# Kernel optimization log

Measured on AMD Instinct MI355X. Metric: run time of the kernel, lower is better.

Reference implementation:

```python
import jax, jax.numpy as jnp
import numpy as np

TAU = 2.0      # spikingjelly MultiStepLIFNode default tau
VTH = 1.0      # default v_threshold
ALPHA = 4.0    # default Sigmoid surrogate alpha
EPS = 1e-5     # BatchNorm eps

# --- STE sign for binarized conv weights (Binarize.apply, det mode, scale=1) ---
@jax.custom_vjp
def ste_sign(x):
    return jnp.sign(x)

def _ss_fwd(x):
    return jnp.sign(x), None

def _ss_bwd(_, g):
    return (g,)

ste_sign.defvjp(_ss_fwd, _ss_bwd)

# --- Heaviside spike with sigmoid surrogate gradient ---
@jax.custom_vjp
def spike_fn(x):
    return (x >= 0.0).astype(x.dtype)

def _sp_fwd(x):
    return (x >= 0.0).astype(x.dtype), x

def _sp_bwd(x, g):
    s = jax.nn.sigmoid(ALPHA * x)
    return (g * ALPHA * s * (1.0 - s),)

spike_fn.defvjp(_sp_fwd, _sp_bwd)

def lif(x):
    # x: [T,B,C,H,W]; LIF with v_reset=None (soft reset), decay_input=True,
    # detach_reset=True (stop_gradient on the reset term).
    def step(v, xt):
        v = v + (xt - v) / TAU
        s = spike_fn(v - VTH)
        v = v - jax.lax.stop_gradient(s) * VTH
        return v, s
    v0 = jnp.zeros_like(x[0])
    _, spikes = jax.lax.scan(step, v0, x)
    return spikes

def conv3x3(x, w, groups=1):
    # x: [N,C,H,W], w: [O, C//groups, 3, 3], stride 1, pad 1
    return jax.lax.conv_general_dilated(
        x, w, window_strides=(1, 1), padding=((1, 1), (1, 1)),
        dimension_numbers=('NCHW', 'OIHW', 'NCHW'),
        feature_group_count=groups)

def setup_inputs() -> dict:
    key = jax.random.key(0)
    k1, k2, k3 = jax.random.split(key, 3)
    x = jax.random.normal(k1, (4, 8, 256, 64, 64), dtype=jnp.float32)
    w1 = jax.random.normal(k2, (192, 256, 3, 3), dtype=jnp.float32) * 0.05
    gamma = jnp.ones((192,), dtype=jnp.float32)
    beta = jnp.zeros((192,), dtype=jnp.float32)
    w2 = jax.random.normal(k3, (320, 48, 3, 3), dtype=jnp.float32) * 0.05
    return {'x': x, 'w1': w1, 'gamma': gamma, 'beta': beta, 'w2': w2}

def reference(x, w1, gamma, beta, w2):
    T, B, C, H, W = x.shape
    s = lif(x).reshape(T * B, C, H, W)          # spikes, flatten(0,1)
    y = conv3x3(s, w1)                          # conv1 (bias=False)
    # BatchNorm2d in training mode: batch stats over (N,H,W), biased var
    mean = y.mean(axis=(0, 2, 3))
    var = y.var(axis=(0, 2, 3))
    yb = (y - mean[None, :, None, None]) * jax.lax.rsqrt(var + EPS)[None, :, None, None]
    yb = yb * gamma[None, :, None, None] + beta[None, :, None, None]
    hidden = yb.shape[1]
    x1 = yb.reshape(T, B, hidden, H, W)
    z = conv3x3(yb, ste_sign(w2), groups=4)     # binarized-weight conv, groups=4
    x2 = z.reshape(T, B, -1, H, W)
    return jnp.concatenate((x1, x2), axis=2)    # [T,B,output_size,H,W]
```

## Files before the change

kernel.cpp:

```cpp
#include <hip/hip_runtime.h>

typedef __bf16 bf16x8 __attribute__((ext_vector_type(8)));
typedef float f32x4 __attribute__((ext_vector_type(4)));

#define DEV static __device__ __forceinline__

DEV ushort f2bf(float f) {
  unsigned u = __builtin_bit_cast(unsigned, f);
  u = (u + 0x7FFFu + ((u >> 16) & 1u)) >> 16;
  return (ushort)u;
}
DEV float bf2f(ushort h) {
  unsigned u = ((unsigned)h) << 16;
  return __builtin_bit_cast(float, u);
}
DEV void gll16(const void* g, void* l) {
  __builtin_amdgcn_global_load_lds((const __attribute__((address_space(1))) void*)g,
                                   (__attribute__((address_space(3))) void*)l, 16, 0, 0);
}

#define Y_OFF      71368704ull
#define WR1_OFF    121700352ull
#define WR2_OFF    122585088ull
#define STATS_OFF  122953728ull
#define ZERO_OFF   122955264ull
#define PART_OFF   122959360ull

DEV void border_px(int p, int& h, int& w) {
  if (p < 66)       { h = 0;       w = p; }
  else if (p < 132) { h = 65;      w = p - 66; }
  else if (p < 196) { h = p - 131; w = 0; }
  else              { h = p - 195; w = 65; }
}
__global__ void halo1_kernel(ushort* __restrict__ S) {
  const int idx = blockIdx.x * 256 + threadIdx.x;
  const int n = idx / 16640, r = idx % 16640;
  const int p = r >> 6, c4 = r & 63;
  int h, w; border_px(p, h, w);
  ushort4 z; z.x = 0; z.y = 0; z.z = 0; z.w = 0;
  *(ushort4*)&S[((size_t)((n * 66 + h) * 66 + w) << 8) + c4 * 4] = z;
}
__global__ void halo2_kernel(ushort* __restrict__ Yb) {
  const int idx = blockIdx.x * 256 + threadIdx.x;
  const int n = idx / 12480, r = idx % 12480;
  const int p = r / 48, c4 = r % 48;
  int h, w; border_px(p, h, w);
  ushort4 z; z.x = 0; z.y = 0; z.z = 0; z.w = 0;
  *(ushort4*)&Yb[(size_t)((n * 66 + h) * 66 + w) * 192 + c4 * 4] = z;
}

__global__ __launch_bounds__(256) void lif_kernel(const float* __restrict__ x,
                                                  ushort* __restrict__ S) {
  const int bi = blockIdx.x;
  const int jq = bi >> 9;
  const int b  = (bi >> 6) & 7;
  const int h  = bi & 63;
  const int tid = threadIdx.x;
  const int w0 = (tid & 15) << 2;
  const int cg = (tid >> 4) + (jq << 4);
  const int c0 = cg << 2;

  float v[4][4];
#pragma unroll
  for (int a = 0; a < 4; ++a)
#pragma unroll
    for (int k = 0; k < 4; ++k) v[a][k] = 0.f;

#pragma unroll
  for (int t = 0; t < 4; ++t) {
    const int n = t * 8 + b;
    ushort sp[4][4];
#pragma unroll
    for (int a = 0; a < 4; ++a) {
      const float4 xv = *(const float4*)(x + ((size_t)(n * 256 + c0 + a) << 12) + (h << 6) + w0);
      const float xa[4] = {xv.x, xv.y, xv.z, xv.w};
#pragma unroll
      for (int k = 0; k < 4; ++k) {
        v[a][k] += (xa[k] - v[a][k]) * 0.5f;
        const bool s = v[a][k] >= 1.0f;
        sp[a][k] = s ? (ushort)0x3F80 : (ushort)0;
        v[a][k] -= s ? 1.0f : 0.0f;
      }
    }
#pragma unroll
    for (int k = 0; k < 4; ++k) {
      ushort4 o4; o4.x = sp[0][k]; o4.y = sp[1][k]; o4.z = sp[2][k]; o4.w = sp[3][k];
      *(ushort4*)(S + ((size_t)((n * 66 + h + 1) * 66 + (w0 + k + 1)) << 8) + c0) = o4;
    }
  }
}

__global__ void prep_w1_kernel(const float* __restrict__ w1, ushort* __restrict__ Wr1) {
  const int idx = blockIdx.x * 256 + threadIdx.x;
  const int pos = idx / 49152, r = idx % 49152;
  const int o = r >> 8, c = r & 255;
  Wr1[idx] = f2bf(w1[(o * 256 + c) * 9 + pos]);
}
__global__ void prep_w2_kernel(const float* __restrict__ w2, ushort* __restrict__ Wr2) {
  const int idx = blockIdx.x * 256 + threadIdx.x;
  const int gp = idx / 5120, r = idx % 5120;
  const int o = r >> 6, c = r & 63;
  const int g = gp / 9, pos = gp % 9;
  float v = 0.f;
  if (c < 48) {
    const float wv = w2[((g * 80 + o) * 48 + c) * 9 + pos];
    v = (wv > 0.f) ? 1.f : ((wv < 0.f) ? -1.f : 0.f);
  }
  Wr2[idx] = f2bf(v);
}

__global__ __launch_bounds__(256, 2) void conv1_kernel(const ushort* __restrict__ S,
                                                       const ushort* __restrict__ Wr1,
                                                       ushort* __restrict__ Y,
                                                       float* __restrict__ Pp) {
  __shared__ ushort ldsA[2][12288];
  __shared__ ushort ldsB[2][8192];
  const int tid = threadIdx.x;
  const int l = tid & 63, wv = tid >> 6;
  const int wrow = wv >> 1, wcol = wv & 1;
  const int col = l & 15, quad = l >> 4;
  const int bid = ((blockIdx.x & 7) << 7) | (blockIdx.x >> 3);
  const int pxb = bid << 7;
  const int n = pxb >> 12;
  const int h0 = (pxb >> 6) & 63;
  const int n66h0 = n * 66 + h0;

  int goA[6], loA[6];
#pragma unroll
  for (int ii = 0; ii < 6; ++ii) {
    const int s = ii * 256 + tid;
    const int kc = s / 768, r = s % 768;
    const int row = r >> 2, op = r & 3;
    const int ol = (op - (row >> 1)) & 3;
    goA[ii] = row * 256 + kc * 32 + ol * 8;
    loA[ii] = s * 8;
  }
  int goB[4], loB[4];
#pragma unroll
  for (int ii = 0; ii < 4; ++ii) {
    const int s = ii * 256 + tid;
    const int kc = s >> 9, r = s & 511;
    const int pxl = r >> 2, op = r & 3;
    const int ol = (op - (pxl >> 1)) & 3;
    goB[ii] = ((pxl >> 6) * 66 + (pxl & 63)) * 256 + kc * 32 + ol * 8;
    loB[ii] = s * 8;
  }
  int offA[6], offB[4];
#pragma unroll
  for (int i = 0; i < 6; ++i) {
    const int row = wrow * 96 + i * 16 + col;
    offA[i] = row * 32 + (((quad + (row >> 1)) & 3) << 3);
  }
#pragma unroll
  for (int j = 0; j < 4; ++j) {
    const int row = wcol * 64 + j * 16 + col;
    offB[j] = row * 32 + (((quad + (row >> 1)) & 3) << 3);
  }

  f32x4 acc[6][4];
#pragma unroll
  for (int i = 0; i < 6; ++i)
#pragma unroll
    for (int j = 0; j < 4; ++j) acc[i][j] = (f32x4){0.f, 0.f, 0.f, 0.f};

  auto stage = [&](int it2, int buf) {
    const int pos = it2 >> 2, cc = it2 & 3;
    const int kh = pos / 3, kw = pos - 3 * kh;
    const int c0 = cc << 6;
    const int uA = pos * 49152 + c0;
    const int uB = ((n66h0 + kh) * 66 + kw) * 256 + c0;
#pragma unroll
    for (int ii = 0; ii < 6; ++ii)
      gll16(Wr1 + uA + goA[ii], &ldsA[buf][loA[ii]]);
#pragma unroll
    for (int ii = 0; ii < 4; ++ii)
      gll16(S + uB + goB[ii], &ldsB[buf][loB[ii]]);
  };

  auto computeTile = [&](int buf) {
#pragma unroll
    for (int kc = 0; kc < 2; ++kc) {
      bf16x8 bf[4];
#pragma unroll
      for (int j = 0; j < 4; ++j)
        bf[j] = *(const bf16x8*)&ldsB[buf][kc * 4096 + offB[j]];
#pragma unroll
      for (int i = 0; i < 6; ++i) {
        const bf16x8 af = *(const bf16x8*)&ldsA[buf][kc * 6144 + offA[i]];
#pragma unroll
        for (int j = 0; j < 4; ++j)
          acc[i][j] = __builtin_amdgcn_mfma_f32_16x16x32_bf16(af, bf[j], acc[i][j], 0, 0, 0);
      }
    }
  };

  stage(0, 0);
  __syncthreads();
  for (int it = 0; it < 36; it += 2) {
    stage(it + 1, 1);
    computeTile(0);
    __syncthreads();
    if (it + 2 < 36) stage(it + 2, 0);
    computeTile(1);
    __syncthreads();
  }

#pragma unroll
  for (int i = 0; i < 6; ++i) {
    const int o = wrow * 96 + i * 16 + quad * 4;
#pragma unroll
    for (int j = 0; j < 4; ++j) {
      const int px = pxb + wcol * 64 + j * 16 + col;
      ushort4 st;
      st.x = f2bf(acc[i][j].x); st.y = f2bf(acc[i][j].y);
      st.z = f2bf(acc[i][j].z); st.w = f2bf(acc[i][j].w);
      *(ushort4*)&Y[px * 192 + o] = st;
    }
  }
#pragma unroll
  for (int i = 0; i < 6; ++i) {
    float s[4], q[4];
#pragma unroll
    for (int k = 0; k < 4; ++k) { s[k] = 0.f; q[k] = 0.f; }
#pragma unroll
    for (int j = 0; j < 4; ++j)
#pragma unroll
      for (int k = 0; k < 4; ++k) {
        const float v = acc[i][j][k];
        s[k] += v; q[k] += v * v;
      }
#pragma unroll
    for (int m = 1; m < 16; m <<= 1)
#pragma unroll
      for (int k = 0; k < 4; ++k) {
        s[k] += __shfl_xor(s[k], m, 64);
        q[k] += __shfl_xor(q[k], m, 64);
      }
    if (col == 0) {
      const int oc = wrow * 96 + i * 16 + quad * 4;
      const int slot = (int)blockIdx.x * 2 + wcol;
#pragma unroll
      for (int k = 0; k < 4; ++k) {
        Pp[(oc + k) * 2048 + slot] = s[k];
        Pp[(192 + oc + k) * 2048 + slot] = q[k];
      }
    }
  }
}

__global__ void reduce_stats_kernel(const float* __restrict__ Pp, float* __restrict__ stats) {
  const int r = blockIdx.x, t = threadIdx.x;
  const float4 a = *(const float4*)&Pp[r * 2048 + t * 8];
  const float4 b = *(const float4*)&Pp[r * 2048 + t * 8 + 4];
  float s = a.x + a.y + a.z + a.w + b.x + b.y + b.z + b.w;
#pragma unroll
  for (int m = 32; m; m >>= 1) s += __shfl_xor(s, m, 64);
  __shared__ float ls[4];
  if ((t & 63) == 0) ls[t >> 6] = s;
  __syncthreads();
  if (t == 0) stats[r] = ls[0] + ls[1] + ls[2] + ls[3];
}

__global__ void bn_kernel(const ushort* __restrict__ Y, const float* __restrict__ stats,
                          const float* __restrict__ gamma, const float* __restrict__ beta,
                          float* __restrict__ out, ushort* __restrict__ Yb) {
  __shared__ float lds[13056];
  const int tid = threadIdx.x;
  const int n = blockIdx.x >> 6, h = blockIdx.x & 63;
  const int cq = tid % 48, wsub = tid / 48;
  const int c0 = cq * 4;
  float a[4], bb[4];
#pragma unroll
  for (int j = 0; j < 4; ++j) {
    const int c = c0 + j;
    const float mean = stats[c] * (1.f / 131072.f);
    const float var = stats[192 + c] * (1.f / 131072.f) - mean * mean;
    const float r = rsqrtf(var + 1e-5f);
    a[j] = gamma[c] * r;
    bb[j] = beta[c] - mean * a[j];
  }
  const int pxrow = n * 4096 + h * 64;
  for (int i = 0; i < 16; ++i) {
    const int w = i * 4 + wsub;
    const ushort4 yv = *(const ushort4*)&Y[(pxrow + w) * 192 + c0];
    float f[4];
    f[0] = a[0] * bf2f(yv.x) + bb[0];
    f[1] = a[1] * bf2f(yv.y) + bb[1];
    f[2] = a[2] * bf2f(yv.z) + bb[2];
    f[3] = a[3] * bf2f(yv.w) + bb[3];
    ushort4 ob;
    ob.x = f2bf(f[0]); ob.y = f2bf(f[1]); ob.z = f2bf(f[2]); ob.w = f2bf(f[3]);
    *(ushort4*)&Yb[(size_t)((n * 66 + h + 1) * 66 + (w + 1)) * 192 + c0] = ob;
#pragma unroll
    for (int j = 0; j < 4; ++j) lds[(c0 + j) * 68 + w] = f[j];
  }
  __syncthreads();
  const int w4 = (tid & 15) << 2, cz = tid >> 4;
  for (int i = 0; i < 16; ++i) {
    const int c = cz * 16 + i;
    const float4 v = *(const float4*)&lds[c * 68 + w4];
    *(float4*)&out[((size_t)(n * 512 + c) << 12) + h * 64 + w4] = v;
  }
}

__global__ __launch_bounds__(256) void conv2_kernel(const ushort* __restrict__ Yb,
                                                    const ushort* __restrict__ Wr2,
                                                    const ushort* __restrict__ zb,
                                                    float* __restrict__ out) {
  __shared__ ushort ldsA[16384];
  __shared__ ushort ldsB[6144];
  const int tid = threadIdx.x;
  const int l = tid & 63, wv = tid >> 6;
  const int col = l & 15, quad = l >> 4;
  const int g = blockIdx.y;
  const int g48 = g * 48;
  const int bid = ((blockIdx.x & 7) << 6) | (blockIdx.x >> 3);
  const int pxb = bid << 8;
  const int n = pxb >> 12;
  const int h0 = (pxb >> 6) & 63;
  const int n66h0 = n * 66 + h0;

  int hrA[8], wA[8], cA[8], vA[8], loA[8];
#pragma unroll
  for (int ii = 0; ii < 8; ++ii) {
    const int s = ii * 256 + tid;
    const int kc = s >> 10, r = s & 1023;
    const int pxl = r >> 2, op = r & 3;
    const int ol = (op - (pxl >> 1)) & 3;
    hrA[ii] = pxl >> 6; wA[ii] = pxl & 63;
    const int c = kc * 32 + ol * 8;
    cA[ii] = c; vA[ii] = (c < 48);
    loA[ii] = s * 8;
  }
  int gB[3], vB[3], loB[3];
#pragma unroll
  for (int ii = 0; ii < 3; ++ii) {
    const int s = ii * 256 + tid;
    const int kc = s / 384, r = s % 384;
    const int row = r >> 2, op = r & 3;
    const int ol = (op - (row >> 1)) & 3;
    vB[ii] = (row < 80);
    gB[ii] = row * 64 + kc * 32 + ol * 8;
    loB[ii] = s * 8;
  }
  int offA[4], offB[5];
#pragma unroll
  for (int i = 0; i < 4; ++i) {
    const int row = wv * 64 + i * 16 + col;
    offA[i] = row * 32 + (((quad + (row >> 1)) & 3) << 3);
  }
#pragma unroll
  for (int j = 0; j < 5; ++j) {
    const int row = j * 16 + col;
    offB[j] = row * 32 + (((quad + (row >> 1)) & 3) << 3);
  }

  f32x4 acc[4][5];
#pragma unroll
  for (int i = 0; i < 4; ++i)
#pragma unroll
    for (int j = 0; j < 5; ++j) acc[i][j] = (f32x4){0.f, 0.f, 0.f, 0.f};

  for (int pos = 0; pos < 9; ++pos) {
    const int kh = pos / 3, kw = pos - 3 * kh;
    const int wbase = (g * 9 + pos) * 5120;
    __syncthreads();
#pragma unroll
    for (int ii = 0; ii < 8; ++ii) {
      const ushort* p = vA[ii]
        ? Yb + (size_t)((n66h0 + hrA[ii] + kh) * 66 + wA[ii] + kw) * 192 + g48 + cA[ii]
        : zb;
      gll16(p, &ldsA[loA[ii]]);
    }
#pragma unroll
    for (int ii = 0; ii < 3; ++ii) {
      const ushort* p = vB[ii] ? Wr2 + wbase + gB[ii] : zb;
      gll16(p, &ldsB[loB[ii]]);
    }
    __syncthreads();
#pragma unroll
    for (int kc = 0; kc < 2; ++kc) {
      bf16x8 bw[5];
#pragma unroll
      for (int j = 0; j < 5; ++j)
        bw[j] = *(const bf16x8*)&ldsB[kc * 3072 + offB[j]];
#pragma unroll
      for (int i = 0; i < 4; ++i) {
        const bf16x8 af = *(const bf16x8*)&ldsA[kc * 8192 + offA[i]];
#pragma unroll
        for (int j = 0; j < 5; ++j)
          acc[i][j] = __builtin_amdgcn_mfma_f32_16x16x32_bf16(af, bw[j], acc[i][j], 0, 0, 0);
      }
    }
  }
#pragma unroll
  for (int i = 0; i < 4; ++i) {
    const int pxl = (pxb & 4095) + wv * 64 + i * 16 + quad * 4;
#pragma unroll
    for (int j = 0; j < 5; ++j) {
      const int o = 192 + g * 80 + j * 16 + col;
      float4 v4;
      v4.x = acc[i][j].x; v4.y = acc[i][j].y; v4.z = acc[i][j].z; v4.w = acc[i][j].w;
      *(float4*)&out[((size_t)(n * 512 + o) << 12) + pxl] = v4;
    }
  }
}

extern "C" void kernel_launch(void* const* d_in, const int* in_sizes, int n_in,
                              void* d_out, int out_size, void* d_ws, size_t ws_size,
                              hipStream_t stream) {
  const float* x     = (const float*)d_in[0];
  const float* w1    = (const float*)d_in[1];
  const float* gamma = (const float*)d_in[2];
  const float* beta  = (const float*)d_in[3];
  const float* w2    = (const float*)d_in[4];
  float* out = (float*)d_out;
  char* ws = (char*)d_ws;

  ushort* S   = (ushort*)ws;
  ushort* Yb  = (ushort*)ws;
  ushort* Y   = (ushort*)(ws + Y_OFF);
  ushort* Wr1 = (ushort*)(ws + WR1_OFF);
  ushort* Wr2 = (ushort*)(ws + WR2_OFF);
  float* stats = (float*)(ws + STATS_OFF);
  const ushort* zb = (const ushort*)(ws + ZERO_OFF);
  float* Pp = (float*)(ws + PART_OFF);

  hipMemsetAsync(ws + ZERO_OFF, 0, 4096, stream);
  hipLaunchKernelGGL(prep_w1_kernel, dim3(1728), dim3(256), 0, stream, w1, Wr1);
  hipLaunchKernelGGL(prep_w2_kernel, dim3(720), dim3(256), 0, stream, w2, Wr2);
  hipLaunchKernelGGL(halo1_kernel, dim3(2080), dim3(256), 0, stream, S);
  hipLaunchKernelGGL(lif_kernel, dim3(2048), dim3(256), 0, stream, x, S);
  hipLaunchKernelGGL(conv1_kernel, dim3(1024), dim3(256), 0, stream, S, Wr1, Y, Pp);
  hipLaunchKernelGGL(reduce_stats_kernel, dim3(384), dim3(256), 0, stream, Pp, stats);
  hipLaunchKernelGGL(halo2_kernel, dim3(1560), dim3(256), 0, stream, Yb);
  hipLaunchKernelGGL(bn_kernel, dim3(2048), dim3(192), 0, stream, Y, stats, gamma, beta, out, Yb);
  hipLaunchKernelGGL(conv2_kernel, dim3(512, 4), dim3(256), 0, stream, Yb, Wr2, zb, out);
}
```

Baseline: 615.0 us.

## Double-buffer conv2 LDS loads and halve pixel tile to raise occupancy

The grouped conv2 kernel now uses two LDS buffers so the global-to-LDS loads for the next 3x3 tap are issued while MFMAs run on the current one, dropping one barrier per tap. The pixel tile per block shrinks from 256 to 128, the grid doubles, launch bounds ask for two blocks per CU, and address math is precomputed into flat offsets. In exchange, weight tiles are reloaded twice as often per output, and there is less MFMA work per barrier.

```diff
diff --git a/kernel.cpp b/kernel.cpp
--- a/kernel.cpp
+++ b/kernel.cpp
@@ -303,36 +303,38 @@
   }
 }
 
-__global__ __launch_bounds__(256) void conv2_kernel(const ushort* __restrict__ Yb,
-                                                    const ushort* __restrict__ Wr2,
-                                                    const ushort* __restrict__ zb,
-                                                    float* __restrict__ out) {
-  __shared__ ushort ldsA[16384];
-  __shared__ ushort ldsB[6144];
+__global__ __launch_bounds__(256, 2) void conv2_kernel(const ushort* __restrict__ Yb,
+                                                       const ushort* __restrict__ Wr2,
+                                                       const ushort* __restrict__ zb,
+                                                       float* __restrict__ out) {
+  __shared__ ushort ldsA[2][8192];
+  __shared__ ushort ldsB[2][6144];
   const int tid = threadIdx.x;
   const int l = tid & 63, wv = tid >> 6;
   const int col = l & 15, quad = l >> 4;
   const int g = blockIdx.y;
   const int g48 = g * 48;
-  const int bid = ((blockIdx.x & 7) << 6) | (blockIdx.x >> 3);
-  const int pxb = bid << 8;
+  const int bid = ((blockIdx.x & 7) << 7) | (blockIdx.x >> 3);
+  const int pxb = bid << 7;
   const int n = pxb >> 12;
   const int h0 = (pxb >> 6) & 63;
   const int n66h0 = n * 66 + h0;
 
-  int hrA[8], wA[8], cA[8], vA[8], loA[8];
-#pragma unroll
-  for (int ii = 0; ii < 8; ++ii) {
+  int goA[4], loA[4];
+  bool vA[4];
+#pragma unroll
+  for (int ii = 0; ii < 4; ++ii) {
     const int s = ii * 256 + tid;
-    const int kc = s >> 10, r = s & 1023;
+    const int kc = s >> 9, r = s & 511;
     const int pxl = r >> 2, op = r & 3;
     const int ol = (op - (pxl >> 1)) & 3;
-    hrA[ii] = pxl >> 6; wA[ii] = pxl & 63;
     const int c = kc * 32 + ol * 8;
-    cA[ii] = c; vA[ii] = (c < 48);
+    vA[ii] = (c < 48);
+    goA[ii] = ((pxl >> 6) * 66 + (pxl & 63)) * 192 + c;
     loA[ii] = s * 8;
   }
-  int gB[3], vB[3], loB[3];
+  int gB[3], loB[3];
+  bool vB[3];
 #pragma unroll
   for (int ii = 0; ii < 3; ++ii) {
     const int s = ii * 256 + tid;
@@ -343,10 +345,10 @@
     gB[ii] = row * 64 + kc * 32 + ol * 8;
     loB[ii] = s * 8;
   }
-  int offA[4], offB[5];
-#pragma unroll
-  for (int i = 0; i < 4; ++i) {
-    const int row = wv * 64 + i * 16 + col;
+  int offA[2], offB[5];
+#pragma unroll
+  for (int i = 0; i < 2; ++i) {
+    const int row = wv * 32 + i * 16 + col;
     offA[i] = row * 32 + (((quad + (row >> 1)) & 3) << 3);
   }
 #pragma unroll
@@ -355,47 +357,60 @@
     offB[j] = row * 32 + (((quad + (row >> 1)) & 3) << 3);
   }
 
-  f32x4 acc[4][5];
-#pragma unroll
-  for (int i = 0; i < 4; ++i)
+  f32x4 acc[2][5];
+#pragma unroll
+  for (int i = 0; i < 2; ++i)
 #pragma unroll
     for (int j = 0; j < 5; ++j) acc[i][j] = (f32x4){0.f, 0.f, 0.f, 0.f};
 
-  for (int pos = 0; pos < 9; ++pos) {
+  auto stage = [&](int pos, int buf) {
     const int kh = pos / 3, kw = pos - 3 * kh;
+    const int uA = ((n66h0 + kh) * 66 + kw) * 192 + g48;
     const int wbase = (g * 9 + pos) * 5120;
-    __syncthreads();
-#pragma unroll
-    for (int ii = 0; ii < 8; ++ii) {
-      const ushort* p = vA[ii]
-        ? Yb + (size_t)((n66h0 + hrA[ii] + kh) * 66 + wA[ii] + kw) * 192 + g48 + cA[ii]
-        : zb;
-      gll16(p, &ldsA[loA[ii]]);
+#pragma unroll
+    for (int ii = 0; ii < 4; ++ii) {
+      const ushort* p = vA[ii] ? Yb + uA + goA[ii] : zb;
+      gll16(p, &ldsA[buf][loA[ii]]);
     }
 #pragma unroll
     for (int ii = 0; ii < 3; ++ii) {
       const ushort* p = vB[ii] ? Wr2 + wbase + gB[ii] : zb;
-      gll16(p, &ldsB[loB[ii]]);
-    }
-    __syncthreads();
+      gll16(p, &ldsB[buf][loB[ii]]);
+    }
+  };
+
+  auto computeTile = [&](int buf) {
 #pragma unroll
     for (int kc = 0; kc < 2; ++kc) {
       bf16x8 bw[5];
 #pragma unroll
       for (int j = 0; j < 5; ++j)
-        bw[j] = *(const bf16x8*)&ldsB[kc * 3072 + offB[j]];
-#pragma unroll
-      for (int i = 0; i < 4; ++i) {
-        const bf16x8 af = *(const bf16x8*)&ldsA[kc * 8192 + offA[i]];
+        bw[j] = *(const bf16x8*)&ldsB[buf][kc * 3072 + offB[j]];
+#pragma unroll
+      for (int i = 0; i < 2; ++i) {
+        const bf16x8 af = *(const bf16x8*)&ldsA[buf][kc * 4096 + offA[i]];
 #pragma unroll
         for (int j = 0; j < 5; ++j)
           acc[i][j] = __builtin_amdgcn_mfma_f32_16x16x32_bf16(af, bw[j], acc[i][j], 0, 0, 0);
       }
     }
-  }
-#pragma unroll
-  for (int i = 0; i < 4; ++i) {
-    const int pxl = (pxb & 4095) + wv * 64 + i * 16 + quad * 4;
+  };
+
+  stage(0, 0);
+  __syncthreads();
+  for (int p = 0; p < 8; p += 2) {
+    stage(p + 1, 1);
+    computeTile(0);
+    __syncthreads();
+    stage(p + 2, 0);
+    computeTile(1);
+    __syncthreads();
+  }
+  computeTile(0);
+
+#pragma unroll
+  for (int i = 0; i < 2; ++i) {
+    const int pxl = (pxb & 4095) + wv * 32 + i * 16 + quad * 4;
 #pragma unroll
     for (int j = 0; j < 5; ++j) {
       const int o = 192 + g * 80 + j * 16 + col;
@@ -435,5 +450,5 @@
   hipLaunchKernelGGL(reduce_stats_kernel, dim3(384), dim3(256), 0, stream, Pp, stats);
   hipLaunchKernelGGL(halo2_kernel, dim3(1560), dim3(256), 0, stream, Yb);
   hipLaunchKernelGGL(bn_kernel, dim3(2048), dim3(192), 0, stream, Y, stats, gamma, beta, out, Yb);
-  hipLaunchKernelGGL(conv2_kernel, dim3(512, 4), dim3(256), 0, stream, Yb, Wr2, zb, out);
-}
+  hipLaunchKernelGGL(conv2_kernel, dim3(1024, 4), dim3(256), 0, stream, Yb, Wr2, zb, out);
+}
```

Result: slower. 631.5 us (+2.7%).
